# Kernel tuning notes

Measured on AMD Instinct MI355X. Metric: run time of the kernel, lower is better.

## Reference

```python
import jax, jax.numpy as jnp
import numpy as np

B, C, H, W = 4, 256, 64, 64
C8, C2 = C // 8, C // 2


def _conv(x, w, b):
    # NCHW conv with SAME padding
    y = jax.lax.conv_general_dilated(x, w, (1, 1), 'SAME',
                                     dimension_numbers=('NCHW', 'OIHW', 'NCHW'))
    return y + b[None, :, None, None]


def _bn(x, s, bi, m, v):
    # eval-mode batchnorm, eps matches torch default 1e-5
    inv = jax.lax.rsqrt(v + 1e-5)
    return (x - m[None, :, None, None]) * (inv * s)[None, :, None, None] + bi[None, :, None, None]


def setup_inputs() -> dict:
    ks = jax.random.split(jax.random.key(0), 8)
    return {
        'x': jax.random.normal(ks[0], (B, C, H, W), jnp.float32),
        'q_w': jax.random.normal(ks[1], (C8, C, 3, 3), jnp.float32) * 0.02,
        'q_b': jnp.zeros((C8,), jnp.float32),
        'q_bn_s': jnp.ones((C8,), jnp.float32),
        'q_bn_b': jnp.zeros((C8,), jnp.float32),
        'q_bn_m': jnp.zeros((C8,), jnp.float32),
        'q_bn_v': jnp.ones((C8,), jnp.float32),
        'k_w': jax.random.normal(ks[2], (C8, C, 3, 3), jnp.float32) * 0.02,
        'k_b': jnp.zeros((C8,), jnp.float32),
        'k_bn_s': jnp.ones((C8,), jnp.float32),
        'k_bn_b': jnp.zeros((C8,), jnp.float32),
        'k_bn_m': jnp.zeros((C8,), jnp.float32),
        'k_bn_v': jnp.ones((C8,), jnp.float32),
        'v_w': jax.random.normal(ks[3], (C, C), jnp.float32) * 0.02,
        'v_b': jnp.zeros((C,), jnp.float32),
        'gamma': jnp.full((1,), 0.5, jnp.float32),
        'c_w1': jax.random.normal(ks[4], (C2, C), jnp.float32) * 0.02,
        'c_b1': jnp.zeros((C2,), jnp.float32),
        'c_w2': jax.random.normal(ks[5], (C, C2), jnp.float32) * 0.02,
        'c_b2': jnp.zeros((C,), jnp.float32),
        's_vw': jax.random.normal(ks[6], (C, C), jnp.float32) * 0.02,
        's_vb': jnp.zeros((C,), jnp.float32),
        's_cw': jax.random.normal(ks[7], (1, 2, 3, 3), jnp.float32) * 0.1,
        's_cb': jnp.zeros((1,), jnp.float32),
        's_bn_s': jnp.ones((1,), jnp.float32),
        's_bn_b': jnp.zeros((1,), jnp.float32),
        's_bn_m': jnp.zeros((1,), jnp.float32),
        's_bn_v': jnp.ones((1,), jnp.float32),
    }


def reference(x, q_w, q_b, q_bn_s, q_bn_b, q_bn_m, q_bn_v,
              k_w, k_b, k_bn_s, k_bn_b, k_bn_m, k_bn_v,
              v_w, v_b, gamma, c_w1, c_b1, c_w2, c_b2,
              s_vw, s_vb, s_cw, s_cb, s_bn_s, s_bn_b, s_bn_m, s_bn_v):
    Bn, Cn, Hn, Wn = x.shape
    HW = Hn * Wn

    # ---- SelfAttention branch ----
    q = jax.nn.relu(_bn(_conv(x, q_w, q_b), q_bn_s, q_bn_b, q_bn_m, q_bn_v)).reshape(Bn, -1, HW)  # [B,C8,HW]
    k = jax.nn.relu(_bn(_conv(x, k_w, k_b), k_bn_s, k_bn_b, k_bn_m, k_bn_v)).reshape(Bn, -1, HW)  # [B,C8,HW]
    aff = jax.nn.softmax(jnp.einsum('bcn,bcm->bnm', q, k), axis=-1)  # [B,HW,HW]
    v = (jnp.einsum('bchw,oc->bohw', x, v_w) + v_b[None, :, None, None]).reshape(Bn, Cn, HW)
    wts = jnp.einsum('bcm,bnm->bcn', v, aff).reshape(Bn, Cn, Hn, Wn)
    selfA = gamma * wts + x

    # ---- Channel mean/max attention ----
    def fc(s):  # s: [B,C]
        h = jax.nn.relu(s @ c_w1.T + c_b1)
        return h @ c_w2.T + c_b2

    gate = jax.nn.sigmoid(fc(x.mean((2, 3))) + fc(x.max((2, 3))))  # [B,C]
    channelA = x * gate[:, :, None, None]

    # ---- Spatial mean/max attention ----
    v2 = jnp.einsum('bchw,oc->bohw', x, s_vw) + s_vb[None, :, None, None]  # [B,C,H,W]
    sm = jnp.stack([v2.max(1), v2.mean(1)], axis=1)  # [B,2,H,W]
    a = _bn(_conv(sm, s_cw, s_cb), s_bn_s, s_bn_b, s_bn_m, s_bn_v)  # [B,1,H,W]
    a = jax.nn.softmax(a[:, 0], axis=-1)  # [B,H,W], softmax over W
    spatialA = jnp.einsum('bchw,bwk->bchk', x, a)  # batched matmul, needs H==W

    return selfA + channelA + spatialA
```

## Files before the change

kernel.cpp:

```cpp
#include <hip/hip_runtime.h>
#include <math.h>

#define NB 4
#define NC 256
#define NHW 4096
#define NC8 32
#define NC2 128

typedef unsigned short u16;
typedef __attribute__((ext_vector_type(8))) short s8v;
typedef __attribute__((ext_vector_type(4))) short s4v;
typedef __attribute__((ext_vector_type(4))) float f4v;

__device__ __forceinline__ u16 f2bf(float x) {
    unsigned int u = __builtin_bit_cast(unsigned int, x);
    u += 0x7FFFu + ((u >> 16) & 1u);
    return (u16)(u >> 16);
}
__device__ __forceinline__ float bf2f(u16 h) {
    unsigned int u = ((unsigned int)h) << 16;
    return __builtin_bit_cast(float, u);
}
__device__ __forceinline__ s8v ld_sp(const u16* p) {
    s4v a = *(const s4v*)p;
    s4v b = *(const s4v*)(p + 4);
    return __builtin_shufflevector(a, b, 0, 1, 2, 3, 4, 5, 6, 7);
}

#define MFMA16(a, b, c) __builtin_amdgcn_mfma_f32_16x16x32_bf16((a), (b), (c), 0, 0, 0)

__global__ __launch_bounds__(256) void k_conv_qk(
    const float* __restrict__ x,
    const float* __restrict__ qw, const float* __restrict__ kw,
    float* __restrict__ part)
{
    __shared__ float plane[2][64 * 65];
    const int cog = blockIdx.x;
    const int cic = blockIdx.y;
    const int b   = blockIdx.z;
    const int t   = threadIdx.x;
    const int co0 = cog * 4;
    const bool isq = co0 < NC8;
    const int oc0 = isq ? co0 : co0 - NC8;
    const float* wsel = isq ? qw : kw;
    const int ci0 = cic * 64;
    const int r  = t >> 2;
    const int c0 = (t & 3) * 16;
    float acc[4][16];
#pragma unroll
    for (int j = 0; j < 4; ++j)
#pragma unroll
        for (int q = 0; q < 16; ++q) acc[j][q] = 0.f;

    const float* xb = x + (size_t)b * NC * NHW;
    float4 pf[4];
    {
        const float4* src = (const float4*)(xb + (size_t)ci0 * NHW);
#pragma unroll
        for (int u = 0; u < 4; ++u) pf[u] = src[t + 256 * u];
    }
    for (int ci = ci0; ci < ci0 + 64; ++ci) {
        const int cur = ci & 1;
#pragma unroll
        for (int u = 0; u < 4; ++u) {
            int g  = (t + 256 * u) << 2;
            int rr = g >> 6, cc = g & 63;
            float* p = &plane[cur][rr * 65 + cc];
            p[0] = pf[u].x; p[1] = pf[u].y; p[2] = pf[u].z; p[3] = pf[u].w;
        }
        __syncthreads();
        if (ci + 1 < ci0 + 64) {
            const float4* src = (const float4*)(xb + (size_t)(ci + 1) * NHW);
#pragma unroll
            for (int u = 0; u < 4; ++u) pf[u] = src[t + 256 * u];
        }
        float w9[4][9];
#pragma unroll
        for (int j = 0; j < 4; ++j)
#pragma unroll
            for (int u = 0; u < 9; ++u)
                w9[j][u] = wsel[((size_t)(oc0 + j) * NC + ci) * 9 + u];
#pragma unroll
        for (int dy = 0; dy < 3; ++dy) {
            int rr = r + dy - 1;
            if (rr >= 0 && rr <= 63) {
                const float* row = &plane[cur][rr * 65];
                float tv[18];
#pragma unroll
                for (int jj = 0; jj < 18; ++jj) {
                    int cc = c0 + jj - 1;
                    tv[jj] = (cc >= 0 && cc < 64) ? row[cc] : 0.f;
                }
#pragma unroll
                for (int j = 0; j < 4; ++j) {
                    float wa = w9[j][dy * 3 + 0], wb = w9[j][dy * 3 + 1], wc = w9[j][dy * 3 + 2];
#pragma unroll
                    for (int q = 0; q < 16; ++q)
                        acc[j][q] += wa * tv[q] + wb * tv[q + 1] + wc * tv[q + 2];
                }
            }
        }
        __syncthreads();
    }
    float* pp = part + (((size_t)(cic * 4 + b) * 64 + co0) * NHW) + r * 64 + c0;
#pragma unroll
    for (int j = 0; j < 4; ++j)
#pragma unroll
        for (int q4 = 0; q4 < 4; ++q4) {
            float4 o;
            o.x = acc[j][q4 * 4 + 0]; o.y = acc[j][q4 * 4 + 1];
            o.z = acc[j][q4 * 4 + 2]; o.w = acc[j][q4 * 4 + 3];
            *(float4*)(pp + (size_t)j * NHW + q4 * 4) = o;
        }
}

__global__ __launch_bounds__(256) void k_qk_finish(
    const float* __restrict__ part,
    const float* __restrict__ qb, const float* __restrict__ qbs, const float* __restrict__ qbb,
    const float* __restrict__ qbm, const float* __restrict__ qbv,
    const float* __restrict__ kb, const float* __restrict__ kbs, const float* __restrict__ kbb,
    const float* __restrict__ kbm, const float* __restrict__ kbv,
    u16* __restrict__ qh, u16* __restrict__ ql,
    u16* __restrict__ kh, u16* __restrict__ kl)
{
    const int t = threadIdx.x;
    const int b = blockIdx.y;
    const int n = blockIdx.x * 64 + (t & 63);
    const int coq = t >> 6;
    const int cb2 = coq * 16;
    float s[16];
#pragma unroll
    for (int j = 0; j < 16; ++j) s[j] = 0.f;
#pragma unroll
    for (int cic = 0; cic < 4; ++cic)
#pragma unroll
        for (int j = 0; j < 16; ++j)
            s[j] += part[(((size_t)(cic * 4 + b)) * 64 + cb2 + j) * NHW + n];
    const bool isq = coq < 2;
    u16 hi[16], lo[16];
#pragma unroll
    for (int j = 0; j < 16; ++j) {
        int oc = (coq & 1) * 16 + j;
        float cbv = isq ? qb[oc]  : kb[oc];
        float sv  = isq ? qbs[oc] : kbs[oc];
        float bbv = isq ? qbb[oc] : kbb[oc];
        float mv  = isq ? qbm[oc] : kbm[oc];
        float vv  = isq ? qbv[oc] : kbv[oc];
        float inv = rsqrtf(vv + 1e-5f);
        float scale = inv * sv;
        float shift = (cbv - mv) * scale + bbv;
        float y = fmaxf(s[j] * scale + shift, 0.f);
        hi[j] = f2bf(y);
        lo[j] = f2bf(y - bf2f(hi[j]));
    }
    u16* dh = isq ? qh : kh;
    u16* dl = isq ? ql : kl;
    size_t base = ((size_t)b * NHW + n) * 32 + (coq & 1) * 16;
    uint4 ph0, ph1, pl0, pl1;
    ph0.x = (unsigned)hi[0]  | ((unsigned)hi[1]  << 16);
    ph0.y = (unsigned)hi[2]  | ((unsigned)hi[3]  << 16);
    ph0.z = (unsigned)hi[4]  | ((unsigned)hi[5]  << 16);
    ph0.w = (unsigned)hi[6]  | ((unsigned)hi[7]  << 16);
    ph1.x = (unsigned)hi[8]  | ((unsigned)hi[9]  << 16);
    ph1.y = (unsigned)hi[10] | ((unsigned)hi[11] << 16);
    ph1.z = (unsigned)hi[12] | ((unsigned)hi[13] << 16);
    ph1.w = (unsigned)hi[14] | ((unsigned)hi[15] << 16);
    pl0.x = (unsigned)lo[0]  | ((unsigned)lo[1]  << 16);
    pl0.y = (unsigned)lo[2]  | ((unsigned)lo[3]  << 16);
    pl0.z = (unsigned)lo[4]  | ((unsigned)lo[5]  << 16);
    pl0.w = (unsigned)lo[6]  | ((unsigned)lo[7]  << 16);
    pl1.x = (unsigned)lo[8]  | ((unsigned)lo[9]  << 16);
    pl1.y = (unsigned)lo[10] | ((unsigned)lo[11] << 16);
    pl1.z = (unsigned)lo[12] | ((unsigned)lo[13] << 16);
    pl1.w = (unsigned)lo[14] | ((unsigned)lo[15] << 16);
    *(uint4*)&dh[base]     = ph0;
    *(uint4*)&dh[base + 8] = ph1;
    *(uint4*)&dl[base]     = pl0;
    *(uint4*)&dl[base + 8] = pl1;
}

__global__ __launch_bounds__(256) void k_gemm_vv2(
    const float* __restrict__ x,
    const float* __restrict__ vw, const float* __restrict__ vb,
    const float* __restrict__ sw, const float* __restrict__ sb,
    float* __restrict__ v2T, u16* __restrict__ vhi, u16* __restrict__ vlo)
{
    __shared__ float Ax[16 * 68];
    __shared__ float Bw1[16 * 68];
    __shared__ float Bw2[16 * 68];
    const int t  = threadIdx.x;
    const int n0 = blockIdx.x * 64;
    const int o0 = blockIdx.y * 64;
    const int b  = blockIdx.z;
    const int ni = t & 15, oi = t >> 4;
    float a1[4][4], a2[4][4];
#pragma unroll
    for (int i = 0; i < 4; ++i)
#pragma unroll
        for (int j = 0; j < 4; ++j) { a1[i][j] = 0.f; a2[i][j] = 0.f; }

    const int sk  = t >> 4;
    const int sf  = t & 15;
    const int so  = t & 63;
    const int skq = t >> 6;
    const float* xb = x + ((size_t)b * NC) * NHW + n0;

    float4 ax = *(const float4*)(xb + (size_t)sk * NHW + sf * 4);
    float4 f1 = *(const float4*)(vw + (size_t)(o0 + so) * NC + skq * 4);
    float4 f2 = *(const float4*)(sw + (size_t)(o0 + so) * NC + skq * 4);

    for (int c0 = 0; c0 < NC; c0 += 16) {
        *(float4*)&Ax[sk * 68 + sf * 4] = ax;
        Bw1[(skq * 4 + 0) * 68 + so] = f1.x;
        Bw1[(skq * 4 + 1) * 68 + so] = f1.y;
        Bw1[(skq * 4 + 2) * 68 + so] = f1.z;
        Bw1[(skq * 4 + 3) * 68 + so] = f1.w;
        Bw2[(skq * 4 + 0) * 68 + so] = f2.x;
        Bw2[(skq * 4 + 1) * 68 + so] = f2.y;
        Bw2[(skq * 4 + 2) * 68 + so] = f2.z;
        Bw2[(skq * 4 + 3) * 68 + so] = f2.w;
        __syncthreads();
        if (c0 + 16 < NC) {
            ax = *(const float4*)(xb + (size_t)(c0 + 16 + sk) * NHW + sf * 4);
            f1 = *(const float4*)(vw + (size_t)(o0 + so) * NC + c0 + 16 + skq * 4);
            f2 = *(const float4*)(sw + (size_t)(o0 + so) * NC + c0 + 16 + skq * 4);
        }
#pragma unroll
        for (int k = 0; k < 16; ++k) {
            float4 af = *(const float4*)&Ax[k * 68 + ni * 4];
            float4 g1 = *(const float4*)&Bw1[k * 68 + oi * 4];
            float4 g2 = *(const float4*)&Bw2[k * 68 + oi * 4];
            const float* ap = (const float*)&af;
            const float* p1 = (const float*)&g1;
            const float* p2 = (const float*)&g2;
#pragma unroll
            for (int i = 0; i < 4; ++i)
#pragma unroll
                for (int j = 0; j < 4; ++j) {
                    a1[i][j] += ap[i] * p1[j];
                    a2[i][j] += ap[i] * p2[j];
                }
        }
        __syncthreads();
    }
    float vb4[4], sb4[4];
#pragma unroll
    for (int j = 0; j < 4; ++j) { vb4[j] = vb[o0 + oi * 4 + j]; sb4[j] = sb[o0 + oi * 4 + j]; }
#pragma unroll
    for (int i = 0; i < 4; ++i) {
        size_t idx = ((size_t)b * NHW + n0 + ni * 4 + i) * NC + o0 + oi * 4;
        float4 o2v;
        o2v.x = a2[i][0] + sb4[0]; o2v.y = a2[i][1] + sb4[1];
        o2v.z = a2[i][2] + sb4[2]; o2v.w = a2[i][3] + sb4[3];
        *(float4*)&v2T[idx] = o2v;
    }
#pragma unroll
    for (int j = 0; j < 4; ++j) {
        u16 h[4], l[4];
#pragma unroll
        for (int i = 0; i < 4; ++i) {
            float y = a1[i][j] + vb4[j];
            h[i] = f2bf(y);
            l[i] = f2bf(y - bf2f(h[i]));
        }
        size_t vi = ((size_t)b * NC + o0 + oi * 4 + j) * NHW + n0 + ni * 4;
        uint2 uh, ul;
        uh.x = (unsigned)h[0] | ((unsigned)h[1] << 16);
        uh.y = (unsigned)h[2] | ((unsigned)h[3] << 16);
        ul.x = (unsigned)l[0] | ((unsigned)l[1] << 16);
        ul.y = (unsigned)l[2] | ((unsigned)l[3] << 16);
        *(uint2*)&vhi[vi] = uh;
        *(uint2*)&vlo[vi] = ul;
    }
}

__global__ __launch_bounds__(256) void k_reduce_v2(const float* __restrict__ v2T,
                                                   float* __restrict__ smo)
{
    const int t = threadIdx.x;
    const int lane = t & 63, wv = t >> 6;
    const int row = blockIdx.x * 4 + wv;
    float4 f = ((const float4*)(v2T + (size_t)row * NC))[lane];
    float mx = fmaxf(fmaxf(f.x, f.y), fmaxf(f.z, f.w));
    float sm = f.x + f.y + f.z + f.w;
#pragma unroll
    for (int off = 32; off; off >>= 1) {
        mx = fmaxf(mx, __shfl_down(mx, off));
        sm += __shfl_down(sm, off);
    }
    if (lane == 0) {
        int b = row >> 12, n = row & 4095;
        smo[((size_t)b * 2 + 0) * NHW + n] = mx;
        smo[((size_t)b * 2 + 1) * NHW + n] = sm * (1.f / NC);
    }
}

__global__ __launch_bounds__(256) void k_spatial(
    const float* __restrict__ smo, const float* __restrict__ scw,
    const float* __restrict__ scb, const float* __restrict__ sbs,
    const float* __restrict__ sbb2, const float* __restrict__ sbm,
    const float* __restrict__ sbv, float* __restrict__ Amat)
{
    __shared__ float ch[2][64 * 68];
    __shared__ float lg[64 * 68];
    const int t = threadIdx.x;
    const int b = blockIdx.x;
#pragma unroll
    for (int u = 0; u < 8; ++u) {
        int g  = t + 256 * u;
        int c  = g >> 10, gi = g & 1023;
        int row = gi >> 4, col4 = (gi & 15) * 4;
        float4 f = ((const float4*)(smo + ((size_t)b * 2 + c) * NHW))[gi];
        *(float4*)&ch[c][row * 68 + col4] = f;
    }
    __syncthreads();
    float w9[2][9];
#pragma unroll
    for (int ic = 0; ic < 2; ++ic)
#pragma unroll
        for (int j = 0; j < 9; ++j) w9[ic][j] = scw[ic * 9 + j];
    float A0, Bsh;
    {
        float inv = rsqrtf(sbv[0] + 1e-5f);
        A0  = inv * sbs[0];
        Bsh = (scb[0] - sbm[0]) * A0 + sbb2[0];
    }
#pragma unroll
    for (int u = 0; u < 16; ++u) {
        int px = t + 256 * u;
        int h = px >> 6, w = px & 63;
        float acc = 0.f;
#pragma unroll
        for (int ic = 0; ic < 2; ++ic)
#pragma unroll
            for (int dy = 0; dy < 3; ++dy) {
                int rr = h + dy - 1;
                if (rr < 0 || rr > 63) continue;
#pragma unroll
                for (int dx = 0; dx < 3; ++dx) {
                    int cc = w + dx - 1;
                    if (cc < 0 || cc > 63) continue;
                    acc += w9[ic][dy * 3 + dx] * ch[ic][rr * 68 + cc];
                }
            }
        lg[h * 68 + w] = acc * A0 + Bsh;
    }
    __syncthreads();
    if (t < 64) {
        float M = -INFINITY;
        for (int k2 = 0; k2 < 64; ++k2) M = fmaxf(M, lg[t * 68 + k2]);
        float L = 0.f;
        for (int k2 = 0; k2 < 64; ++k2) L += __expf(lg[t * 68 + k2] - M);
        float rli = 1.f / L;
        for (int k2 = 0; k2 < 64; ++k2)
            Amat[(size_t)b * NHW + t * 64 + k2] = __expf(lg[t * 68 + k2] - M) * rli;
    }
}

__global__ __launch_bounds__(256) void k_xstats(const float* __restrict__ x,
                                                float* __restrict__ smean,
                                                float* __restrict__ smax)
{
    const int t = threadIdx.x;
    const int c = blockIdx.x, b = blockIdx.y;
    const float* row = x + ((size_t)b * NC + c) * NHW;
    float s = 0.f, m = -INFINITY;
#pragma unroll
    for (int u = 0; u < 4; ++u) {
        float4 f = ((const float4*)row)[t + 256 * u];
        s += f.x + f.y + f.z + f.w;
        m = fmaxf(m, fmaxf(fmaxf(f.x, f.y), fmaxf(f.z, f.w)));
    }
    __shared__ float red[8];
    const int lane = t & 63, wv = t >> 6;
#pragma unroll
    for (int off = 32; off; off >>= 1) {
        s += __shfl_down(s, off);
        m = fmaxf(m, __shfl_down(m, off));
    }
    if (lane == 0) { red[wv] = s; red[4 + wv] = m; }
    __syncthreads();
    if (t == 0) {
        float S = red[0] + red[1] + red[2] + red[3];
        float M = fmaxf(fmaxf(red[4], red[5]), fmaxf(red[6], red[7]));
        smean[b * NC + c] = S * (1.f / NHW);
        smax[b * NC + c]  = M;
    }
}

__global__ __launch_bounds__(256) void k_gate(
    const float* __restrict__ smean, const float* __restrict__ smax,
    const float* __restrict__ w1, const float* __restrict__ b1,
    const float* __restrict__ w2, const float* __restrict__ b2,
    float* __restrict__ gate)
{
    __shared__ float smL[256], sxL[256], hL[256];
    const int t = threadIdx.x;
    const int b = blockIdx.x;
    smL[t] = smean[b * NC + t];
    sxL[t] = smax[b * NC + t];
    __syncthreads();
    {
        const int j = t & 127;
        const float* in = (t < 128) ? smL : sxL;
        const float* wr = w1 + (size_t)j * NC;
        float acc = b1[j];
        for (int c = 0; c < NC; c += 4) {
            float4 f = *(const float4*)(wr + c);
            acc += f.x * in[c] + f.y * in[c + 1] + f.z * in[c + 2] + f.w * in[c + 3];
        }
        hL[t] = fmaxf(acc, 0.f);
    }
    __syncthreads();
    {
        const float* wr = w2 + (size_t)t * NC2;
        float acc = 2.f * b2[t];
        for (int j = 0; j < NC2; j += 4) {
            float4 f = *(const float4*)(wr + j);
            acc += f.x * (hL[j]     + hL[128 + j])
                 + f.y * (hL[j + 1] + hL[129 + j])
                 + f.z * (hL[j + 2] + hL[130 + j])
                 + f.w * (hL[j + 3] + hL[131 + j]);
        }
        gate[b * NC + t] = 1.f / (1.f + __expf(-acc));
    }
}

__global__ __launch_bounds__(64) void k_softstats(
    const u16* __restrict__ qh, const u16* __restrict__ ql,
    const u16* __restrict__ kh, const u16* __restrict__ kl,
    float* __restrict__ mx, float* __restrict__ rl)
{
    const int t  = threadIdx.x;
    const int li = t & 15, g = t >> 4;
    const int n0 = blockIdx.x * 16;
    const int b  = blockIdx.y;
    const size_t qoff = ((size_t)b * NHW + n0 + li) * 32 + g * 8;
    const s8v qfh = *(const s8v*)&qh[qoff];
    const s8v qfl = *(const s8v*)&ql[qoff];
    const size_t kb0 = ((size_t)b * NHW + li) * 32 + g * 8;
    s8v ka0 = *(const s8v*)&kh[kb0];
    s8v ka1 = *(const s8v*)&kh[kb0 + 512];
    s8v la0 = *(const s8v*)&kl[kb0];
    s8v la1 = *(const s8v*)&kl[kb0 + 512];
    float mrun = -INFINITY, lrun = 0.f;
    for (int it = 0; it < 128; ++it) {
        f4v c0 = {0.f, 0.f, 0.f, 0.f}, c1 = {0.f, 0.f, 0.f, 0.f};
        c0 = MFMA16(ka0, qfh, c0); c0 = MFMA16(ka0, qfl, c0); c0 = MFMA16(la0, qfh, c0);
        c1 = MFMA16(ka1, qfh, c1); c1 = MFMA16(ka1, qfl, c1); c1 = MFMA16(la1, qfh, c1);
        if (it + 1 < 128) {
            size_t o = kb0 + (size_t)(it + 1) * 1024;
            ka0 = *(const s8v*)&kh[o];
            ka1 = *(const s8v*)&kh[o + 512];
            la0 = *(const s8v*)&kl[o];
            la1 = *(const s8v*)&kl[o + 512];
        }
        float tmax = fmaxf(fmaxf(fmaxf(c0[0], c0[1]), fmaxf(c0[2], c0[3])),
                           fmaxf(fmaxf(c1[0], c1[1]), fmaxf(c1[2], c1[3])));
        tmax = fmaxf(tmax, __shfl_xor(tmax, 16));
        tmax = fmaxf(tmax, __shfl_xor(tmax, 32));
        float nm = fmaxf(mrun, tmax);
        float ls = 0.f;
#pragma unroll
        for (int r = 0; r < 4; ++r) ls += __expf(c0[r] - nm);
#pragma unroll
        for (int r = 0; r < 4; ++r) ls += __expf(c1[r] - nm);
        ls += __shfl_xor(ls, 16);
        ls += __shfl_xor(ls, 32);
        lrun = lrun * __expf(mrun - nm) + ls;
        mrun = nm;
    }
    if (g == 0) {
        mx[(size_t)b * NHW + n0 + li] = mrun;
        rl[(size_t)b * NHW + n0 + li] = 1.f / lrun;
    }
}

__global__ __launch_bounds__(512, 4) void k_flash(
    const u16* __restrict__ qh, const u16* __restrict__ ql,
    const u16* __restrict__ kh, const u16* __restrict__ kl,
    const u16* __restrict__ vhi, const u16* __restrict__ vlo,
    const float* __restrict__ mx, const float* __restrict__ rl,
    u16* __restrict__ w)
{
    __shared__ __align__(16) u16 Sk[2][2][32 * 40];
    __shared__ __align__(16) u16 Sp[2][4][16 * 36];
    const int t = threadIdx.x;
    const int bid = blockIdx.x;
    const int v   = (bid & 7) * 128 + (bid >> 3);
    const int n0  = (v & 63) * 64;
    const int mh  = (v >> 6) & 3;
    const int b   = v >> 8;
    const int mbase = mh * 1024;
    const int li = t & 15, g = (t >> 4) & 3, wv = t >> 6;
    const bool qkrole = wv < 4;

    s8v qfh = {0,0,0,0,0,0,0,0}, qfl = {0,0,0,0,0,0,0,0};
    float mxv = 0.f, rlv = 0.f;
    if (qkrole) {
        const size_t qoff = ((size_t)b * NHW + n0 + wv * 16 + li) * 32 + g * 8;
        qfh = *(const s8v*)&qh[qoff];
        qfl = *(const s8v*)&ql[qoff];
        mxv = mx[(size_t)b * NHW + n0 + wv * 16 + li];
        rlv = rl[(size_t)b * NHW + n0 + wv * 16 + li];
    }
    const int tid2 = t - 256;
    const int sel  = (tid2 >> 7) & 1;
    const int sidx = tid2 & 127;
    const int smp  = sidx >> 2;
    const int sc8  = (sidx & 3) * 8;
    const u16* ksrc = sel ? kl : kh;
    const size_t kgbase = ((size_t)b * NHW + mbase + smp) * 32 + sc8;
    s8v kreg = {0,0,0,0,0,0,0,0};
    if (!qkrole) {
        kreg = *(const s8v*)&ksrc[kgbase];
        *(s8v*)&Sk[0][sel][smp * 40 + sc8] = kreg;
        kreg = *(const s8v*)&ksrc[kgbase + 1024];
    }
    const size_t vb0 = ((size_t)b * NC + wv * 32 + li) * NHW + mbase + g * 8;
    s8v vfh[2], vfl[2];
#pragma unroll
    for (int ct = 0; ct < 2; ++ct) {
        vfh[ct] = *(const s8v*)&vhi[vb0 + (size_t)ct * 16 * NHW];
        vfl[ct] = *(const s8v*)&vlo[vb0 + (size_t)ct * 16 * NHW];
    }
    f4v acc[4][2];
#pragma unroll
    for (int i = 0; i < 4; ++i)
#pragma unroll
        for (int j = 0; j < 2; ++j) { f4v z = {0.f, 0.f, 0.f, 0.f}; acc[i][j] = z; }

    __syncthreads();

    for (int it = 0; it < 32; ++it) {
        if (qkrole) {
            const u16* skh = &Sk[it & 1][0][0];
            const u16* skl = &Sk[it & 1][1][0];
            s8v ka0 = *(const s8v*)&skh[li * 40 + g * 8];
            s8v ka1 = *(const s8v*)&skh[(16 + li) * 40 + g * 8];
            s8v la0 = *(const s8v*)&skl[li * 40 + g * 8];
            s8v la1 = *(const s8v*)&skl[(16 + li) * 40 + g * 8];
            f4v c0 = {0.f, 0.f, 0.f, 0.f}, c1 = {0.f, 0.f, 0.f, 0.f};
            c0 = MFMA16(ka0, qfh, c0); c0 = MFMA16(ka0, qfl, c0); c0 = MFMA16(la0, qfh, c0);
            c1 = MFMA16(ka1, qfh, c1); c1 = MFMA16(ka1, qfl, c1); c1 = MFMA16(la1, qfh, c1);
            u16 h0[4], h1[4];
#pragma unroll
            for (int r = 0; r < 4; ++r) {
                h0[r] = f2bf(__expf(c0[r] - mxv) * rlv);
                h1[r] = f2bf(__expf(c1[r] - mxv) * rlv);
            }
            u16* sp = &Sp[it & 1][wv][0];
            uint2 uw0, uw1;
            uw0.x = (unsigned)h0[0] | ((unsigned)h0[1] << 16);
            uw0.y = (unsigned)h0[2] | ((unsigned)h0[3] << 16);
            uw1.x = (unsigned)h1[0] | ((unsigned)h1[1] << 16);
            uw1.y = (unsigned)h1[2] | ((unsigned)h1[3] << 16);
            *(uint2*)&sp[li * 36 + g * 4]      = uw0;
            *(uint2*)&sp[li * 36 + 16 + g * 4] = uw1;
        } else {
            *(s8v*)&Sk[(it + 1) & 1][sel][smp * 40 + sc8] = kreg;
            kreg = *(const s8v*)&ksrc[kgbase + (size_t)(it + 2) * 1024];
        }
        asm volatile("s_waitcnt lgkmcnt(0)" ::: "memory");
        __builtin_amdgcn_s_barrier();
        asm volatile("" ::: "memory");
        s8v pa[4];
#pragma unroll
        for (int ng = 0; ng < 4; ++ng)
            pa[ng] = ld_sp(&Sp[it & 1][ng][li * 36 + g * 8]);
#pragma unroll
        for (int ng = 0; ng < 4; ++ng) {
            acc[ng][0] = MFMA16(pa[ng], vfh[0], acc[ng][0]);
            acc[ng][0] = MFMA16(pa[ng], vfl[0], acc[ng][0]);
            acc[ng][1] = MFMA16(pa[ng], vfh[1], acc[ng][1]);
            acc[ng][1] = MFMA16(pa[ng], vfl[1], acc[ng][1]);
        }
        {
            size_t o = vb0 + (size_t)(it + 1) * 32;
#pragma unroll
            for (int ct = 0; ct < 2; ++ct) {
                vfh[ct] = *(const s8v*)&vhi[o + (size_t)ct * 16 * NHW];
                vfl[ct] = *(const s8v*)&vlo[o + (size_t)ct * 16 * NHW];
            }
        }
    }
    u16* wout = w + (size_t)mh * 4194304;
#pragma unroll
    for (int ng = 0; ng < 4; ++ng)
#pragma unroll
        for (int ct = 0; ct < 2; ++ct)
#pragma unroll
            for (int r = 0; r < 4; ++r)
                wout[((size_t)b * NHW + n0 + ng * 16 + g * 4 + r) * NC
                     + wv * 32 + ct * 16 + li] = f2bf(acc[ng][ct][r]);
}

__global__ __launch_bounds__(256) void k_final(
    const float* __restrict__ x, const u16* __restrict__ wp,
    const float* __restrict__ gate,
    const float* __restrict__ Amat, const float* __restrict__ gamma,
    float* __restrict__ out)
{
    __shared__ float As[64 * 65];
    __shared__ float xs[64 * 65];
    const int t = threadIdx.x;
    const int h = blockIdx.x, b = blockIdx.y;
    const float g0 = gamma[0];
    const int kq = t >> 4;
    const int cq = t & 15;
#pragma unroll
    for (int u = 0; u < 4; ++u) {
        int gidx = t + 256 * u;
        int w = gidx >> 4, k4 = (gidx & 15) * 4;
        float4 f = ((const float4*)(Amat + (size_t)b * NHW))[gidx];
        *(float4*)&As[w * 65 + k4] = f;
    }
    for (int ch = 0; ch < 4; ++ch) {
        __syncthreads();
#pragma unroll
        for (int u = 0; u < 4; ++u) {
            int gidx = t + 256 * u;
            int c = gidx >> 4, w4 = (gidx & 15) * 4;
            float4 f = *(const float4*)(x + ((size_t)(b * NC) + ch * 64 + c) * NHW + h * 64 + w4);
            xs[(w4 + 0) * 65 + c] = f.x;
            xs[(w4 + 1) * 65 + c] = f.y;
            xs[(w4 + 2) * 65 + c] = f.z;
            xs[(w4 + 3) * 65 + c] = f.w;
        }
        __syncthreads();
        float acc[4][4];
#pragma unroll
        for (int i = 0; i < 4; ++i)
#pragma unroll
            for (int j = 0; j < 4; ++j) acc[i][j] = 0.f;
        for (int w = 0; w < 64; ++w) {
            float4 av = *(const float4*)&As[w * 65 + kq * 4];
            float4 xv = *(const float4*)&xs[w * 65 + cq * 4];
            const float* ap = (const float*)&av;
            const float* xp = (const float*)&xv;
#pragma unroll
            for (int i = 0; i < 4; ++i)
#pragma unroll
                for (int j = 0; j < 4; ++j)
                    acc[i][j] += xp[i] * ap[j];
        }
        float gt1[4];
#pragma unroll
        for (int i = 0; i < 4; ++i) gt1[i] = 1.f + gate[b * NC + ch * 64 + cq * 4 + i];
#pragma unroll
        for (int j = 0; j < 4; ++j) {
            const int k = kq * 4 + j;
            const int n = h * 64 + k;
            size_t wb = ((size_t)b * NHW + n) * NC + ch * 64 + cq * 4;
            float ws4[4] = {0.f, 0.f, 0.f, 0.f};
#pragma unroll
            for (int m = 0; m < 4; ++m) {
                uint2 uw = *(const uint2*)&wp[(size_t)m * 4194304 + wb];
                ws4[0] += bf2f((u16)(uw.x & 0xffff));
                ws4[1] += bf2f((u16)(uw.x >> 16));
                ws4[2] += bf2f((u16)(uw.y & 0xffff));
                ws4[3] += bf2f((u16)(uw.y >> 16));
            }
#pragma unroll
            for (int i = 0; i < 4; ++i) {
                const int c = ch * 64 + cq * 4 + i;
                const float xv = xs[k * 65 + cq * 4 + i];
                out[((size_t)(b * NC + c)) * NHW + n] = g0 * ws4[i] + xv * gt1[i] + acc[i][j];
            }
        }
    }
}

extern "C" void kernel_launch(void* const* d_in, const int* in_sizes, int n_in,
                              void* d_out, int out_size, void* d_ws, size_t ws_size,
                              hipStream_t stream)
{
    const float* x    = (const float*)d_in[0];
    const float* qw   = (const float*)d_in[1];
    const float* qb   = (const float*)d_in[2];
    const float* qbs  = (const float*)d_in[3];
    const float* qbb  = (const float*)d_in[4];
    const float* qbm  = (const float*)d_in[5];
    const float* qbv  = (const float*)d_in[6];
    const float* kw   = (const float*)d_in[7];
    const float* kb   = (const float*)d_in[8];
    const float* kbs  = (const float*)d_in[9];
    const float* kbb  = (const float*)d_in[10];
    const float* kbm  = (const float*)d_in[11];
    const float* kbv  = (const float*)d_in[12];
    const float* vw   = (const float*)d_in[13];
    const float* vb   = (const float*)d_in[14];
    const float* gm   = (const float*)d_in[15];
    const float* cw1  = (const float*)d_in[16];
    const float* cb1  = (const float*)d_in[17];
    const float* cw2  = (const float*)d_in[18];
    const float* cb2  = (const float*)d_in[19];
    const float* svw  = (const float*)d_in[20];
    const float* svb  = (const float*)d_in[21];
    const float* scw  = (const float*)d_in[22];
    const float* scb  = (const float*)d_in[23];
    const float* sbs  = (const float*)d_in[24];
    const float* sbb  = (const float*)d_in[25];
    const float* sbm  = (const float*)d_in[26];
    const float* sbv  = (const float*)d_in[27];

    float* ws    = (float*)d_ws;
    float* part  = ws;
    float* v2T   = ws + 4194304;
    u16*   wbf   = (u16*)ws;
    u16*   vhi   = (u16*)(ws + 8388608);
    u16*   vlo   = (u16*)(ws + 10485760);
    u16*   qhB   = (u16*)(ws + 12582912);
    u16*   qlB   = (u16*)(ws + 12845056);
    u16*   khB   = (u16*)(ws + 13107200);
    u16*   klB   = (u16*)(ws + 13369344);
    float* mxp   = ws + 13631488;
    float* rlp   = ws + 13647872;
    float* smean = ws + 13664256;
    float* smax  = ws + 13665280;
    float* gate  = ws + 13666304;
    float* smo   = ws + 13667328;
    float* Amat  = ws + 13700096;

    k_conv_qk  <<<dim3(16, 4, NB), 256, 0, stream>>>(x, qw, kw, part);
    k_qk_finish<<<dim3(64, NB),    256, 0, stream>>>(part, qb, qbs, qbb, qbm, qbv,
                                                     kb, kbs, kbb, kbm, kbv,
                                                     qhB, qlB, khB, klB);
    k_gemm_vv2 <<<dim3(64, 4, NB), 256, 0, stream>>>(x, vw, vb, svw, svb, v2T, vhi, vlo);
    k_reduce_v2<<<dim3(4096),      256, 0, stream>>>(v2T, smo);
    k_spatial  <<<dim3(NB),        256, 0, stream>>>(smo, scw, scb, sbs, sbb, sbm, sbv, Amat);
    k_xstats   <<<dim3(NC, NB),    256, 0, stream>>>(x, smean, smax);
    k_gate     <<<dim3(NB),        256, 0, stream>>>(smean, smax, cw1, cb1, cw2, cb2, gate);
    k_softstats<<<dim3(256, NB),   64,  0, stream>>>(qhB, qlB, khB, klB, mxp, rlp);
    k_flash    <<<dim3(1024),      512, 0, stream>>>(qhB, qlB, khB, klB, vhi, vlo,
                                                     mxp, rlp, wbf);
    k_final    <<<dim3(64, NB),    256, 0, stream>>>(x, wbf, gate, Amat, gm,
                                                     (float*)d_out);
}
```

Measured before the change: 504.0 us.

## Stage V tiles through LDS in flash kernel and widen softstats blocks

In the flash kernel, the V hi/lo tiles are now loaded from global memory by the producer waves and staged into a single-buffered LDS tile. Compute waves then read their V fragments from LDS instead of each issuing strided global loads, which is meant to cut redundant, poorly coalesced global traffic. A second barrier per iteration is added to protect the single V buffer, the P scratch stride is padded to 40 for aligned 16-byte reads, and the occupancy hint drops to 2 blocks because of the larger LDS use. The softstats kernel now packs four waves per block instead of one.

After: 515.0 us. 2.2% more time.

```diff
diff --git a/kernel.cpp b/kernel.cpp
--- a/kernel.cpp
+++ b/kernel.cpp
@@ -9,7 +9,6 @@
 
 typedef unsigned short u16;
 typedef __attribute__((ext_vector_type(8))) short s8v;
-typedef __attribute__((ext_vector_type(4))) short s4v;
 typedef __attribute__((ext_vector_type(4))) float f4v;
 
 __device__ __forceinline__ u16 f2bf(float x) {
@@ -20,11 +19,6 @@
 __device__ __forceinline__ float bf2f(u16 h) {
     unsigned int u = ((unsigned int)h) << 16;
     return __builtin_bit_cast(float, u);
-}
-__device__ __forceinline__ s8v ld_sp(const u16* p) {
-    s4v a = *(const s4v*)p;
-    s4v b = *(const s4v*)(p + 4);
-    return __builtin_shufflevector(a, b, 0, 1, 2, 3, 4, 5, 6, 7);
 }
 
 #define MFMA16(a, b, c) __builtin_amdgcn_mfma_f32_16x16x32_bf16((a), (b), (c), 0, 0, 0)
@@ -426,14 +420,15 @@
     }
 }
 
-__global__ __launch_bounds__(64) void k_softstats(
+__global__ __launch_bounds__(256) void k_softstats(
     const u16* __restrict__ qh, const u16* __restrict__ ql,
     const u16* __restrict__ kh, const u16* __restrict__ kl,
     float* __restrict__ mx, float* __restrict__ rl)
 {
-    const int t  = threadIdx.x;
-    const int li = t & 15, g = t >> 4;
-    const int n0 = blockIdx.x * 16;
+    const int t    = threadIdx.x;
+    const int lane = t & 63, wv = t >> 6;
+    const int li = lane & 15, g = lane >> 4;
+    const int n0 = blockIdx.x * 64 + wv * 16;
     const int b  = blockIdx.y;
     const size_t qoff = ((size_t)b * NHW + n0 + li) * 32 + g * 8;
     const s8v qfh = *(const s8v*)&qh[qoff];
@@ -476,15 +471,16 @@
     }
 }
 
-__global__ __launch_bounds__(512, 4) void k_flash(
+__global__ __launch_bounds__(512, 2) void k_flash(
     const u16* __restrict__ qh, const u16* __restrict__ ql,
     const u16* __restrict__ kh, const u16* __restrict__ kl,
     const u16* __restrict__ vhi, const u16* __restrict__ vlo,
     const float* __restrict__ mx, const float* __restrict__ rl,
     u16* __restrict__ w)
 {
+    __shared__ __align__(16) u16 Sv[2][256 * 40];
     __shared__ __align__(16) u16 Sk[2][2][32 * 40];
-    __shared__ __align__(16) u16 Sp[2][4][16 * 36];
+    __shared__ __align__(16) u16 Sp[2][4][16 * 40];
     const int t = threadIdx.x;
     const int bid = blockIdx.x;
     const int v   = (bid & 7) * 128 + (bid >> 3);
@@ -504,6 +500,7 @@
         mxv = mx[(size_t)b * NHW + n0 + wv * 16 + li];
         rlv = rl[(size_t)b * NHW + n0 + wv * 16 + li];
     }
+
     const int tid2 = t - 256;
     const int sel  = (tid2 >> 7) & 1;
     const int sidx = tid2 & 127;
@@ -512,18 +509,23 @@
     const u16* ksrc = sel ? kl : kh;
     const size_t kgbase = ((size_t)b * NHW + mbase + smp) * 32 + sc8;
     s8v kreg = {0,0,0,0,0,0,0,0};
+    s8v vreg[8];
+    size_t vgb[8];
     if (!qkrole) {
-        kreg = *(const s8v*)&ksrc[kgbase];
-        *(s8v*)&Sk[0][sel][smp * 40 + sc8] = kreg;
+#pragma unroll
+        for (int u = 0; u < 8; ++u) {
+            int gi = tid2 + 256 * u;
+            int cc = (gi >> 2) & 255, mc = gi & 3;
+            vgb[u] = ((size_t)b * NC + cc) * NHW + mbase + mc * 8;
+        }
+#pragma unroll
+        for (int u = 0; u < 8; ++u)
+            vreg[u] = *(const s8v*)&((u < 4) ? vhi : vlo)[vgb[u]];
+        s8v k0 = *(const s8v*)&ksrc[kgbase];
+        *(s8v*)&Sk[0][sel][smp * 40 + sc8] = k0;
         kreg = *(const s8v*)&ksrc[kgbase + 1024];
     }
-    const size_t vb0 = ((size_t)b * NC + wv * 32 + li) * NHW + mbase + g * 8;
-    s8v vfh[2], vfl[2];
-#pragma unroll
-    for (int ct = 0; ct < 2; ++ct) {
-        vfh[ct] = *(const s8v*)&vhi[vb0 + (size_t)ct * 16 * NHW];
-        vfl[ct] = *(const s8v*)&vlo[vb0 + (size_t)ct * 16 * NHW];
-    }
+
     f4v acc[4][2];
 #pragma unroll
     for (int i = 0; i < 4; ++i)
@@ -555,10 +557,19 @@
             uw0.y = (unsigned)h0[2] | ((unsigned)h0[3] << 16);
             uw1.x = (unsigned)h1[0] | ((unsigned)h1[1] << 16);
             uw1.y = (unsigned)h1[2] | ((unsigned)h1[3] << 16);
-            *(uint2*)&sp[li * 36 + g * 4]      = uw0;
-            *(uint2*)&sp[li * 36 + 16 + g * 4] = uw1;
+            *(uint2*)&sp[li * 40 + g * 4]      = uw0;
+            *(uint2*)&sp[li * 40 + 16 + g * 4] = uw1;
         } else {
+#pragma unroll
+            for (int u = 0; u < 8; ++u) {
+                int gi = tid2 + 256 * u;
+                int hl = gi >> 10, cc = (gi >> 2) & 255, mc = gi & 3;
+                *(s8v*)&Sv[hl][cc * 40 + mc * 8] = vreg[u];
+            }
             *(s8v*)&Sk[(it + 1) & 1][sel][smp * 40 + sc8] = kreg;
+#pragma unroll
+            for (int u = 0; u < 8; ++u)
+                vreg[u] = *(const s8v*)&((u < 4) ? vhi : vlo)[vgb[u] + (size_t)(it + 1) * 32];
             kreg = *(const s8v*)&ksrc[kgbase + (size_t)(it + 2) * 1024];
         }
         asm volatile("s_waitcnt lgkmcnt(0)" ::: "memory");
@@ -567,22 +578,24 @@
         s8v pa[4];
 #pragma unroll
         for (int ng = 0; ng < 4; ++ng)
-            pa[ng] = ld_sp(&Sp[it & 1][ng][li * 36 + g * 8]);
+            pa[ng] = *(const s8v*)&Sp[it & 1][ng][li * 40 + g * 8];
+        s8v vf[2][2];
+#pragma unroll
+        for (int ct = 0; ct < 2; ++ct) {
+            int cc = wv * 32 + ct * 16 + li;
+            vf[ct][0] = *(const s8v*)&Sv[0][cc * 40 + g * 8];
+            vf[ct][1] = *(const s8v*)&Sv[1][cc * 40 + g * 8];
+        }
 #pragma unroll
         for (int ng = 0; ng < 4; ++ng) {
-            acc[ng][0] = MFMA16(pa[ng], vfh[0], acc[ng][0]);
-            acc[ng][0] = MFMA16(pa[ng], vfl[0], acc[ng][0]);
-            acc[ng][1] = MFMA16(pa[ng], vfh[1], acc[ng][1]);
-            acc[ng][1] = MFMA16(pa[ng], vfl[1], acc[ng][1]);
-        }
-        {
-            size_t o = vb0 + (size_t)(it + 1) * 32;
-#pragma unroll
-            for (int ct = 0; ct < 2; ++ct) {
-                vfh[ct] = *(const s8v*)&vhi[o + (size_t)ct * 16 * NHW];
-                vfl[ct] = *(const s8v*)&vlo[o + (size_t)ct * 16 * NHW];
-            }
-        }
+            acc[ng][0] = MFMA16(pa[ng], vf[0][0], acc[ng][0]);
+            acc[ng][0] = MFMA16(pa[ng], vf[0][1], acc[ng][0]);
+            acc[ng][1] = MFMA16(pa[ng], vf[1][0], acc[ng][1]);
+            acc[ng][1] = MFMA16(pa[ng], vf[1][1], acc[ng][1]);
+        }
+        asm volatile("s_waitcnt lgkmcnt(0)" ::: "memory");
+        __builtin_amdgcn_s_barrier();
+        asm volatile("" ::: "memory");
     }
     u16* wout = w + (size_t)mh * 4194304;
 #pragma unroll
@@ -731,7 +744,7 @@
     k_spatial  <<<dim3(NB),        256, 0, stream>>>(smo, scw, scb, sbs, sbb, sbm, sbv, Amat);
     k_xstats   <<<dim3(NC, NB),    256, 0, stream>>>(x, smean, smax);
     k_gate     <<<dim3(NB),        256, 0, stream>>>(smean, smax, cw1, cb1, cw2, cb2, gate);
-    k_softstats<<<dim3(256, NB),   64,  0, stream>>>(qhB, qlB, khB, klB, mxp, rlp);
+    k_softstats<<<dim3(64, NB),    256, 0, stream>>>(qhB, qlB, khB, klB, mxp, rlp);
     k_flash    <<<dim3(1024),      512, 0, stream>>>(qhB, qlB, khB, klB, vhi, vlo,
                                                      mxp, rlp, wbf);
     k_final    <<<dim3(64, NB),    256, 0, stream>>>(x, wbf, gate, Amat, gm,
```
